# Kernel tuning notes

Measured on AMD Instinct MI355X. Metric: run time of the kernel, lower is better.

Reference implementation:

```python
import jax, jax.numpy as jnp
import numpy as np

# Quantization constants from the original module
X_ZP = -66   # int8 zero point
Y_ZP = 160   # uint8 zero point


def setup_inputs() -> dict:
    key = jax.random.key(0)
    k1, k2 = jax.random.split(key)
    # x: [7, B, M, K] int8 in [-128, 127]
    x = jax.random.randint(k1, (7, 8, 512, 1024), -128, 128, dtype=jnp.int32).astype(jnp.int8)
    # y: [B, K, N] uint8 in [0, 255]
    y = jax.random.randint(k2, (8, 1024, 512), 0, 256, dtype=jnp.int32).astype(jnp.uint8)
    return {
        "x": x,
        "y": y,
        "x_scale": jnp.float32(0.03),
        "y_scale": jnp.float32(0.025),
    }


def reference(x, y, x_scale, y_scale):
    # dequantize_per_tensor: (q - zero_point) * scale
    xf = (x.astype(jnp.float32) - jnp.float32(X_ZP)) * x_scale   # [7, B, M, K]
    yf = (y.astype(jnp.float32) - jnp.float32(Y_ZP)) * y_scale   # [B, K, N]
    # torch.matmul broadcast: [7,B,M,K] @ [B,K,N] -> [7,B,M,N]
    return jnp.einsum('gbmk,bkn->gbmn', xf, yf)
```

## Files before the change

kernel.cpp:

```cpp
#include <hip/hip_runtime.h>
#include <stdint.h>

#define AS1 __attribute__((address_space(1)))
#define AS3 __attribute__((address_space(3)))

typedef int v4i __attribute__((ext_vector_type(4)));

constexpr int G = 7, B = 8, M = 512, N = 512, K = 1024;
constexpr int GBn = G * B;

constexpr size_t X8_BYTES = (size_t)GBn * M * K;
constexpr size_t YT_BYTES = (size_t)B * N * K;
constexpr size_t RS_CNT   = (size_t)GBn * M;
constexpr size_t CS_CNT   = (size_t)B * N;
constexpr size_t WS_NEEDED = X8_BYTES + YT_BYTES + RS_CNT * 4 + CS_CNT * 4;

__global__ __launch_bounds__(256) void transpose_pack_y(const int* __restrict__ y,
                                                        signed char* __restrict__ yt) {
    __shared__ unsigned char tile[64][80];
    int n0 = blockIdx.x * 64;
    int k0 = blockIdx.y * 64;
    int b  = blockIdx.z;
    int t  = threadIdx.x;

    int r  = t >> 2;
    int c0 = (t & 3) * 16;
    const int* src = y + ((size_t)b * K + k0 + r) * N + n0 + c0;
    uint32_t p[4];
#pragma unroll
    for (int q = 0; q < 4; ++q) {
        int4 v = ((const int4*)src)[q];
        p[q] =  (uint32_t)((v.x & 255) ^ 128)
             | ((uint32_t)((v.y & 255) ^ 128) << 8)
             | ((uint32_t)((v.z & 255) ^ 128) << 16)
             | ((uint32_t)((v.w & 255) ^ 128) << 24);
    }
    *(uint4*)&tile[r][c0] = make_uint4(p[0], p[1], p[2], p[3]);
    __syncthreads();

    int nl = t >> 2;
    int kc = (t & 3) * 16;
    uint32_t q[4];
#pragma unroll
    for (int w = 0; w < 4; ++w) {
        uint32_t b0 = tile[kc + w * 4 + 0][nl];
        uint32_t b1 = tile[kc + w * 4 + 1][nl];
        uint32_t b2 = tile[kc + w * 4 + 2][nl];
        uint32_t b3 = tile[kc + w * 4 + 3][nl];
        q[w] = b0 | (b1 << 8) | (b2 << 16) | (b3 << 24);
    }
    *(uint4*)(yt + ((size_t)b * N + n0 + nl) * K + k0 + kc) = make_uint4(q[0], q[1], q[2], q[3]);
}

__device__ __forceinline__ int wave_reduce_sum(int v) {
#pragma unroll
    for (int off = 32; off > 0; off >>= 1) v += __shfl_down(v, off, 64);
    return v;
}

__global__ __launch_bounds__(256) void pack_x_sums(const int* __restrict__ x,
                                                   signed char* __restrict__ x8,
                                                   const signed char* __restrict__ yt,
                                                   int* __restrict__ rowsum,
                                                   int* __restrict__ colsum) {
    int wave = threadIdx.x >> 6, lane = threadIdx.x & 63;
    int row = blockIdx.x * 4 + wave;
    if (row < (int)(GBn * M)) {
        const int* src = x + (size_t)row * K + lane * 16;
        int s = 0;
        uint32_t p[4];
#pragma unroll
        for (int q = 0; q < 4; ++q) {
            int4 v = ((const int4*)src)[q];
            s += v.x + v.y + v.z + v.w;
            p[q] =  (uint32_t)(v.x & 255)
                 | ((uint32_t)(v.y & 255) << 8)
                 | ((uint32_t)(v.z & 255) << 16)
                 | ((uint32_t)(v.w & 255) << 24);
        }
        *(uint4*)(x8 + (size_t)row * K + lane * 16) = make_uint4(p[0], p[1], p[2], p[3]);
        s = wave_reduce_sum(s);
        if (lane == 0) rowsum[row] = s;
    } else {
        int rr = row - (int)(GBn * M);
        uint4 u = *(const uint4*)(yt + (size_t)rr * K + lane * 16);
        uint32_t wds[4] = {u.x, u.y, u.z, u.w};
        int s = 0;
#pragma unroll
        for (int q = 0; q < 4; ++q) {
            uint32_t w = wds[q];
            s += (int)(signed char)(w) + (int)(signed char)(w >> 8)
               + (int)(signed char)(w >> 16) + (int)(signed char)(w >> 24);
        }
        s = wave_reduce_sum(s);
        if (lane == 0) colsum[rr] = s;
    }
}

__global__ __launch_bounds__(256, 4) void gemm_i8(const signed char* __restrict__ x8,
                                                  const signed char* __restrict__ yt,
                                                  const int* __restrict__ rowsum,
                                                  const int* __restrict__ colsum,
                                                  const float* __restrict__ xsp,
                                                  const float* __restrict__ ysp,
                                                  float* __restrict__ out) {
    __shared__ signed char Bs[2][128 * 64];

    int mt = blockIdx.x;
    int nt = blockIdx.y;
    int gb = blockIdx.z;
    int b  = gb & 7;
    int tid = threadIdx.x, wave = tid >> 6, lane = tid & 63;
    int wm = (wave >> 1) * 64, wn = (wave & 1) * 64;
    int fr = lane & 15;
    int q  = lane >> 4;

    int srow  = lane >> 2;
    int sslot = (lane & 3) ^ ((lane >> 3) & 3);
    const signed char* Bb = yt + ((size_t)(b * N + nt * 128 + wave * 16 + srow)) * K + sslot * 16;

    const signed char* Aq = x8 + ((size_t)(gb * M + mt * 128 + wm + fr)) * K + q * 16;

    int fkB = (q ^ ((fr >> 1) & 3)) * 16;

    v4i acc[4][4];
#pragma unroll
    for (int i = 0; i < 4; ++i)
#pragma unroll
        for (int j = 0; j < 4; ++j) acc[i][j] = (v4i){0, 0, 0, 0};

#pragma unroll
    for (int c = 0; c < 2; ++c)
        __builtin_amdgcn_global_load_lds((const AS1 uint32_t*)(Bb + (size_t)c * 64 * K),
                                         (AS3 uint32_t*)(&Bs[0][0] + c * 4096 + wave * 1024), 16, 0, 0);

    for (int step = 0; step < 16; ++step) {
        int k0  = step * 64;
        int cur = step & 1;
        __syncthreads();
        if (step < 15) {
#pragma unroll
            for (int c = 0; c < 2; ++c)
                __builtin_amdgcn_global_load_lds((const AS1 uint32_t*)(Bb + (size_t)c * 64 * K + k0 + 64),
                                                 (AS3 uint32_t*)(&Bs[cur ^ 1][0] + c * 4096 + wave * 1024), 16, 0, 0);
        }
        v4i af[4], bf[4];
#pragma unroll
        for (int i = 0; i < 4; ++i)
            af[i] = *(const v4i*)(Aq + (size_t)i * 16 * K + k0);
#pragma unroll
        for (int j = 0; j < 4; ++j)
            bf[j] = *(const v4i*)(&Bs[cur][0] + (wn + j * 16 + fr) * 64 + fkB);
#pragma unroll
        for (int i = 0; i < 4; ++i)
#pragma unroll
            for (int j = 0; j < 4; ++j)
                acc[i][j] = __builtin_amdgcn_mfma_i32_16x16x64_i8(af[i], bf[j], acc[i][j], 0, 0, 0);
    }

    float s = xsp[0] * ysp[0];
    int colL = lane & 15;
    int rowQ = (lane >> 4) * 4;
    float* outg = out + (size_t)gb * M * N;
    const int* rs = rowsum + gb * M;
    const int* cs = colsum + b * N;
#pragma unroll
    for (int i = 0; i < 4; ++i) {
#pragma unroll
        for (int r = 0; r < 4; ++r) {
            int row_g = mt * 128 + wm + i * 16 + rowQ + r;
            int rsv = rs[row_g];
#pragma unroll
            for (int j = 0; j < 4; ++j) {
                int col_g = nt * 128 + wn + j * 16 + colL;
                int t = acc[i][j][r] - 32 * rsv + 66 * cs[col_g] - 2162688;
                outg[(size_t)row_g * N + col_g] = s * (float)t;
            }
        }
    }
}

__global__ __launch_bounds__(256) void naive_kernel(const int* __restrict__ x,
                                                    const int* __restrict__ y,
                                                    const float* __restrict__ xsp,
                                                    const float* __restrict__ ysp,
                                                    float* __restrict__ out) {
    size_t idx = (size_t)blockIdx.x * 256 + threadIdx.x;
    int n  = (int)(idx & 511);
    int m  = (int)((idx >> 9) & 511);
    int gb = (int)(idx >> 18);
    int b  = gb & 7;
    const int* xr = x + ((size_t)gb * M + m) * K;
    const int* yc = y + (size_t)b * K * N + n;
    int dot = 0, sx = 0, sy = 0;
    for (int k = 0; k < K; ++k) {
        int a = xr[k];
        int c = yc[(size_t)k * N];
        dot += a * c; sx += a; sy += c;
    }
    float s = xsp[0] * ysp[0];
    out[idx] = s * (float)(dot - 160 * sx + 66 * sy - 10813440);
}

extern "C" void kernel_launch(void* const* d_in, const int* in_sizes, int n_in,
                              void* d_out, int out_size, void* d_ws, size_t ws_size,
                              hipStream_t stream) {
    const int*   x  = (const int*)d_in[0];
    const int*   y  = (const int*)d_in[1];
    const float* xs = (const float*)d_in[2];
    const float* ys = (const float*)d_in[3];
    float* out = (float*)d_out;

    if (ws_size < WS_NEEDED) {
        naive_kernel<<<(14680064 + 255) / 256, 256, 0, stream>>>(x, y, xs, ys, out);
        return;
    }

    char* ws = (char*)d_ws;
    signed char* x8 = (signed char*)ws;
    signed char* yt = (signed char*)(ws + X8_BYTES);
    int* rowsum = (int*)(ws + X8_BYTES + YT_BYTES);
    int* colsum = rowsum + RS_CNT;

    transpose_pack_y<<<dim3(N / 64, K / 64, B), 256, 0, stream>>>(y, yt);
    pack_x_sums<<<(GBn * M + CS_CNT) / 4, 256, 0, stream>>>(x, x8, yt, rowsum, colsum);
    gemm_i8<<<dim3(M / 128, N / 128, GBn), 256, 0, stream>>>(x8, yt, rowsum, colsum, xs, ys, out);
}
```

Before: 241.4 us.

## Fuse x int8 packing and row sums into GEMM with 128x256 tiles

```diff
diff --git a/kernel.cpp b/kernel.cpp
--- a/kernel.cpp
+++ b/kernel.cpp
@@ -9,11 +9,9 @@
 constexpr int G = 7, B = 8, M = 512, N = 512, K = 1024;
 constexpr int GBn = G * B;
 
-constexpr size_t X8_BYTES = (size_t)GBn * M * K;
 constexpr size_t YT_BYTES = (size_t)B * N * K;
-constexpr size_t RS_CNT   = (size_t)GBn * M;
 constexpr size_t CS_CNT   = (size_t)B * N;
-constexpr size_t WS_NEEDED = X8_BYTES + YT_BYTES + RS_CNT * 4 + CS_CNT * 4;
+constexpr size_t WS_NEEDED = YT_BYTES + CS_CNT * 4;
 
 __global__ __launch_bounds__(256) void transpose_pack_y(const int* __restrict__ y,
                                                         signed char* __restrict__ yt) {
@@ -52,76 +50,51 @@
     *(uint4*)(yt + ((size_t)b * N + n0 + nl) * K + k0 + kc) = make_uint4(q[0], q[1], q[2], q[3]);
 }
 
-__device__ __forceinline__ int wave_reduce_sum(int v) {
-#pragma unroll
-    for (int off = 32; off > 0; off >>= 1) v += __shfl_down(v, off, 64);
-    return v;
-}
-
-__global__ __launch_bounds__(256) void pack_x_sums(const int* __restrict__ x,
-                                                   signed char* __restrict__ x8,
-                                                   const signed char* __restrict__ yt,
-                                                   int* __restrict__ rowsum,
-                                                   int* __restrict__ colsum) {
+__global__ __launch_bounds__(256) void colsum_y(const signed char* __restrict__ yt,
+                                                int* __restrict__ colsum) {
     int wave = threadIdx.x >> 6, lane = threadIdx.x & 63;
-    int row = blockIdx.x * 4 + wave;
-    if (row < (int)(GBn * M)) {
-        const int* src = x + (size_t)row * K + lane * 16;
-        int s = 0;
-        uint32_t p[4];
-#pragma unroll
-        for (int q = 0; q < 4; ++q) {
-            int4 v = ((const int4*)src)[q];
-            s += v.x + v.y + v.z + v.w;
-            p[q] =  (uint32_t)(v.x & 255)
-                 | ((uint32_t)(v.y & 255) << 8)
-                 | ((uint32_t)(v.z & 255) << 16)
-                 | ((uint32_t)(v.w & 255) << 24);
-        }
-        *(uint4*)(x8 + (size_t)row * K + lane * 16) = make_uint4(p[0], p[1], p[2], p[3]);
-        s = wave_reduce_sum(s);
-        if (lane == 0) rowsum[row] = s;
-    } else {
-        int rr = row - (int)(GBn * M);
-        uint4 u = *(const uint4*)(yt + (size_t)rr * K + lane * 16);
-        uint32_t wds[4] = {u.x, u.y, u.z, u.w};
-        int s = 0;
-#pragma unroll
-        for (int q = 0; q < 4; ++q) {
-            uint32_t w = wds[q];
-            s += (int)(signed char)(w) + (int)(signed char)(w >> 8)
-               + (int)(signed char)(w >> 16) + (int)(signed char)(w >> 24);
-        }
-        s = wave_reduce_sum(s);
-        if (lane == 0) colsum[rr] = s;
-    }
-}
-
-__global__ __launch_bounds__(256, 4) void gemm_i8(const signed char* __restrict__ x8,
+    int rr = blockIdx.x * 4 + wave;
+    uint4 u = *(const uint4*)(yt + (size_t)rr * K + lane * 16);
+    uint32_t wds[4] = {u.x, u.y, u.z, u.w};
+    int s = 0;
+#pragma unroll
+    for (int q = 0; q < 4; ++q) {
+        uint32_t w = wds[q];
+        s += (int)(signed char)(w) + (int)(signed char)(w >> 8)
+           + (int)(signed char)(w >> 16) + (int)(signed char)(w >> 24);
+    }
+#pragma unroll
+    for (int off = 32; off > 0; off >>= 1) s += __shfl_down(s, off, 64);
+    if (lane == 0) colsum[rr] = s;
+}
+
+__global__ __launch_bounds__(512, 4) void gemm_i8(const int* __restrict__ x,
                                                   const signed char* __restrict__ yt,
-                                                  const int* __restrict__ rowsum,
                                                   const int* __restrict__ colsum,
                                                   const float* __restrict__ xsp,
                                                   const float* __restrict__ ysp,
                                                   float* __restrict__ out) {
-    __shared__ signed char Bs[2][128 * 64];
+    __shared__ signed char As[2][128 * 64];
+    __shared__ signed char Bs[2][256 * 64];
+    __shared__ int rsm[128];
 
     int mt = blockIdx.x;
     int nt = blockIdx.y;
     int gb = blockIdx.z;
     int b  = gb & 7;
     int tid = threadIdx.x, wave = tid >> 6, lane = tid & 63;
-    int wm = (wave >> 1) * 64, wn = (wave & 1) * 64;
-    int fr = lane & 15;
-    int q  = lane >> 4;
-
-    int srow  = lane >> 2;
-    int sslot = (lane & 3) ^ ((lane >> 3) & 3);
-    const signed char* Bb = yt + ((size_t)(b * N + nt * 128 + wave * 16 + srow)) * K + sslot * 16;
-
-    const signed char* Aq = x8 + ((size_t)(gb * M + mt * 128 + wm + fr)) * K + q * 16;
-
-    int fkB = (q ^ ((fr >> 1) & 3)) * 16;
+    int wm = (wave >> 2) * 64, wn = (wave & 3) * 64;
+
+    int arow = tid >> 2;
+    const int* xr = x + ((size_t)(gb * M + mt * 128 + arow)) * K + (tid & 3) * 16;
+    int aslot = (tid & 3) ^ ((arow >> 1) & 3);
+    int aoff  = arow * 64 + aslot * 16;
+
+    int bslot = (lane & 3) ^ ((lane >> 3) & 3);
+    const signed char* Bb = yt + ((size_t)(b * N + nt * 256 + wave * 16 + (lane >> 2))) * K + bslot * 16;
+
+    int fr = lane & 15, q = lane >> 4;
+    int fko = (q ^ ((fr >> 1) & 3)) * 16;
 
     v4i acc[4][4];
 #pragma unroll
@@ -129,52 +102,90 @@
 #pragma unroll
         for (int j = 0; j < 4; ++j) acc[i][j] = (v4i){0, 0, 0, 0};
 
+    int rs_part = 0;
+
+    int4 xv[4];
+#pragma unroll
+    for (int h = 0; h < 4; ++h) xv[h] = ((const int4*)xr)[h];
 #pragma unroll
     for (int c = 0; c < 2; ++c)
-        __builtin_amdgcn_global_load_lds((const AS1 uint32_t*)(Bb + (size_t)c * 64 * K),
-                                         (AS3 uint32_t*)(&Bs[0][0] + c * 4096 + wave * 1024), 16, 0, 0);
-
-    for (int step = 0; step < 16; ++step) {
-        int k0  = step * 64;
-        int cur = step & 1;
+        __builtin_amdgcn_global_load_lds((const AS1 uint32_t*)(Bb + (size_t)c * 128 * K),
+                                         (AS3 uint32_t*)(&Bs[0][0] + c * 8192 + wave * 1024), 16, 0, 0);
+    {
+        uint32_t pw[4];
+#pragma unroll
+        for (int h = 0; h < 4; ++h) {
+            int4 v = xv[h];
+            rs_part += v.x + v.y + v.z + v.w;
+            pw[h] =  (uint32_t)(v.x & 255) | ((uint32_t)(v.y & 255) << 8)
+                  | ((uint32_t)(v.z & 255) << 16) | ((uint32_t)(v.w & 255) << 24);
+        }
+        *(uint4*)(&As[0][0] + aoff) = make_uint4(pw[0], pw[1], pw[2], pw[3]);
+    }
+
+    for (int s = 0; s < 16; ++s) {
+        int cur = s & 1;
         __syncthreads();
-        if (step < 15) {
+
+        int4 xn[4];
+        if (s < 15) {
+            const int* xs_ = xr + (s + 1) * 64;
+#pragma unroll
+            for (int h = 0; h < 4; ++h) xn[h] = ((const int4*)xs_)[h];
 #pragma unroll
             for (int c = 0; c < 2; ++c)
-                __builtin_amdgcn_global_load_lds((const AS1 uint32_t*)(Bb + (size_t)c * 64 * K + k0 + 64),
-                                                 (AS3 uint32_t*)(&Bs[cur ^ 1][0] + c * 4096 + wave * 1024), 16, 0, 0);
-        }
+                __builtin_amdgcn_global_load_lds((const AS1 uint32_t*)(Bb + (size_t)c * 128 * K + (s + 1) * 64),
+                                                 (AS3 uint32_t*)(&Bs[cur ^ 1][0] + c * 8192 + wave * 1024), 16, 0, 0);
+        }
+
         v4i af[4], bf[4];
 #pragma unroll
         for (int i = 0; i < 4; ++i)
-            af[i] = *(const v4i*)(Aq + (size_t)i * 16 * K + k0);
+            af[i] = *(const v4i*)(&As[cur][0] + (wm + i * 16 + fr) * 64 + fko);
 #pragma unroll
         for (int j = 0; j < 4; ++j)
-            bf[j] = *(const v4i*)(&Bs[cur][0] + (wn + j * 16 + fr) * 64 + fkB);
+            bf[j] = *(const v4i*)(&Bs[cur][0] + (wn + j * 16 + fr) * 64 + fko);
 #pragma unroll
         for (int i = 0; i < 4; ++i)
 #pragma unroll
             for (int j = 0; j < 4; ++j)
                 acc[i][j] = __builtin_amdgcn_mfma_i32_16x16x64_i8(af[i], bf[j], acc[i][j], 0, 0, 0);
-    }
-
-    float s = xsp[0] * ysp[0];
+
+        if (s < 15) {
+            uint32_t pw[4];
+#pragma unroll
+            for (int h = 0; h < 4; ++h) {
+                int4 v = xn[h];
+                rs_part += v.x + v.y + v.z + v.w;
+                pw[h] =  (uint32_t)(v.x & 255) | ((uint32_t)(v.y & 255) << 8)
+                      | ((uint32_t)(v.z & 255) << 16) | ((uint32_t)(v.w & 255) << 24);
+            }
+            *(uint4*)(&As[cur ^ 1][0] + aoff) = make_uint4(pw[0], pw[1], pw[2], pw[3]);
+        }
+    }
+
+    rs_part += __shfl_down(rs_part, 1, 64);
+    rs_part += __shfl_down(rs_part, 2, 64);
+    if ((lane & 3) == 0) rsm[arow] = rs_part;
+    __syncthreads();
+
+    float sc = xsp[0] * ysp[0];
     int colL = lane & 15;
     int rowQ = (lane >> 4) * 4;
     float* outg = out + (size_t)gb * M * N;
-    const int* rs = rowsum + gb * M;
     const int* cs = colsum + b * N;
 #pragma unroll
     for (int i = 0; i < 4; ++i) {
 #pragma unroll
         for (int r = 0; r < 4; ++r) {
-            int row_g = mt * 128 + wm + i * 16 + rowQ + r;
-            int rsv = rs[row_g];
+            int row_l = wm + i * 16 + rowQ + r;
+            int row_g = mt * 128 + row_l;
+            int rsv = rsm[row_l];
 #pragma unroll
             for (int j = 0; j < 4; ++j) {
-                int col_g = nt * 128 + wn + j * 16 + colL;
+                int col_g = nt * 256 + wn + j * 16 + colL;
                 int t = acc[i][j][r] - 32 * rsv + 66 * cs[col_g] - 2162688;
-                outg[(size_t)row_g * N + col_g] = s * (float)t;
+                outg[(size_t)row_g * N + col_g] = sc * (float)t;
             }
         }
     }
@@ -217,12 +228,10 @@
     }
 
     char* ws = (char*)d_ws;
-    signed char* x8 = (signed char*)ws;
-    signed char* yt = (signed char*)(ws + X8_BYTES);
-    int* rowsum = (int*)(ws + X8_BYTES + YT_BYTES);
-    int* colsum = rowsum + RS_CNT;
+    signed char* yt = (signed char*)ws;
+    int* colsum = (int*)(ws + YT_BYTES);
 
     transpose_pack_y<<<dim3(N / 64, K / 64, B), 256, 0, stream>>>(y, yt);
-    pack_x_sums<<<(GBn * M + CS_CNT) / 4, 256, 0, stream>>>(x, x8, yt, rowsum, colsum);
-    gemm_i8<<<dim3(M / 128, N / 128, GBn), 256, 0, stream>>>(x8, yt, rowsum, colsum, xs, ys, out);
-}
+    colsum_y<<<(B * N) / 4, 256, 0, stream>>>(yt, colsum);
+    gemm_i8<<<dim3(M / 128, N / 256, GBn), 512, 0, stream>>>(x, yt, colsum, xs, ys, out);
+}
```

Measured after the change: 228.3 us. 5.4% less time.
